# Kernel tuning notes

Measured on AMD Instinct MI355X. Metric: run time of the kernel, lower is better.

Reference implementation:

```python
import jax, jax.numpy as jnp
import numpy as np

EMBED_DIM = 768
NUM_HEADS = 12
HEAD_DIM = EMBED_DIM // NUM_HEADS  # 64


def setup_inputs() -> dict:
    key = jax.random.key(0)
    ks = jax.random.split(key, 8)
    B, T, C, H, D = 32, 512, EMBED_DIM, NUM_HEADS, HEAD_DIM
    s = 0.02
    x = jax.random.normal(ks[0], (B, T, C), dtype=jnp.float32)
    # per-head qkv: Linear(C -> 3D) stacked over heads
    Wqkv = jax.random.normal(ks[1], (H, C, 3 * D), dtype=jnp.float32) * s
    bqkv = jax.random.normal(ks[2], (H, 3 * D), dtype=jnp.float32) * s
    # per-head output proj: Linear(D -> C) stacked over heads
    Wph = jax.random.normal(ks[3], (H, D, C), dtype=jnp.float32) * s
    bph = jax.random.normal(ks[4], (H, C), dtype=jnp.float32) * s
    # final proj: Linear(H*C -> C)  (H*C == num_heads*num_heads*head_dim)
    Wproj = jax.random.normal(ks[5], (H * C, C), dtype=jnp.float32) * s
    bproj = jax.random.normal(ks[6], (C,), dtype=jnp.float32) * s
    return {"x": x, "Wqkv": Wqkv, "bqkv": bqkv, "Wph": Wph, "bph": bph,
            "Wproj": Wproj, "bproj": bproj}


def reference(x, Wqkv, bqkv, Wph, bph, Wproj, bproj):
    B, T, C = x.shape
    H, D = NUM_HEADS, HEAD_DIM
    scale = 1.0 / np.sqrt(D).astype(np.float32)
    # batched per-head qkv projection: [B,H,T,3D]
    qkv = jnp.einsum('btc,hcd->bhtd', x, Wqkv) + bqkv[None, :, None, :]
    q, k, v = jnp.split(qkv, 3, axis=-1)  # each [B,H,T,D]
    attn = jnp.einsum('bhtd,bhsd->bhts', q, k) * scale
    sa_probs = jax.nn.softmax(attn, axis=-1)  # [B,H,T,T]
    sa = jnp.einsum('bhts,bhsd->bhtd', sa_probs, v)  # [B,H,T,D]
    # per-head projection D -> C, then concat over heads (head-major order)
    heads_out = jnp.einsum('bhtd,hdc->bhtc', sa, Wph) + bph[None, :, None, :]
    cat = heads_out.transpose(0, 2, 1, 3).reshape(B, T, H * C)
    sa_out = cat @ Wproj + bproj  # [B,T,C]
    return sa_out, sa_probs
```

## Files before the change

### kernel.cpp

```cpp
#include <hip/hip_runtime.h>
#include <stdint.h>

typedef float f32x4 __attribute__((ext_vector_type(4)));
typedef short bf16x8 __attribute__((ext_vector_type(8)));

__device__ __forceinline__ unsigned short f2bf(float f) {
  union { float f; uint32_t u; } v; v.f = f;
  uint32_t r = v.u + 0x7FFFu + ((v.u >> 16) & 1u);
  return (unsigned short)(r >> 16);
}

__device__ __forceinline__ void gload16(const unsigned short* g, unsigned short* l) {
  __builtin_amdgcn_global_load_lds(
      (const __attribute__((address_space(1))) void*)g,
      (__attribute__((address_space(3))) void*)l, 16, 0, 0);
}

__global__ __launch_bounds__(256) void conv_f2b(const float* __restrict__ in,
                                                unsigned short* __restrict__ out, long n) {
  long i = ((long)blockIdx.x * 256 + threadIdx.x) * 4;
  if (i + 3 < n) {
    float4 f = *(const float4*)(in + i);
    ushort4 o;
    o.x = f2bf(f.x); o.y = f2bf(f.y); o.z = f2bf(f.z); o.w = f2bf(f.w);
    *(ushort4*)(out + i) = o;
  }
}

__global__ __launch_bounds__(256) void transpose_f2b(const float* __restrict__ in,
                                                     unsigned short* __restrict__ out,
                                                     int R, int C) {
  __shared__ unsigned short tile[32][33];
  long base = (long)blockIdx.z * R * C;
  in += base; out += base;
  int c0 = blockIdx.x * 32, r0 = blockIdx.y * 32;
  int tx = threadIdx.x & 31, ty = threadIdx.x >> 5;
#pragma unroll
  for (int i = 0; i < 32; i += 8)
    tile[ty + i][tx] = f2bf(in[(long)(r0 + ty + i) * C + c0 + tx]);
  __syncthreads();
#pragma unroll
  for (int i = 0; i < 32; i += 8)
    out[(long)(c0 + ty + i) * R + r0 + tx] = tile[tx][ty + i];
}

__global__ __launch_bounds__(256) void bias_fuse(const float* __restrict__ bph,
                                                 const float* __restrict__ Wproj,
                                                 const float* __restrict__ bproj,
                                                 float* __restrict__ bfused) {
  int j = blockIdx.x * 256 + threadIdx.x;
  int r0 = blockIdx.y * 256;
  float acc = 0.f;
  for (int r = r0; r < r0 + 256; r++)
    acc += bph[r] * Wproj[(long)r * 768 + j];
  if (blockIdx.y == 0) acc += bproj[j];
  atomicAdd(&bfused[j], acc);
}

__device__ __forceinline__ void stage8(const unsigned short* __restrict__ g,
                                       unsigned short* __restrict__ s) {
  *(uint4*)s = *(const uint4*)g;
}

template <typename AT, typename Epi>
__global__ __launch_bounds__(256) void gemm_bt(const AT* __restrict__ A, long asb, int lda,
                                               const unsigned short* __restrict__ Bt, long bsb,
                                               int ldb, int K, Epi epi) {
  __shared__ __align__(16) unsigned short As[64][32];
  __shared__ __align__(16) unsigned short Bs[64][32];
  const int tid = threadIdx.x;
  const int row = tid >> 2;
  const int kc = (tid & 3) * 8;
  const int lane = tid & 63;
  const int w = tid >> 6;
  const int quad = lane >> 4, lr = lane & 15;
  const int bz = blockIdx.z;

  f32x4 acc[4];
#pragma unroll
  for (int i = 0; i < 4; i++) acc[i] = (f32x4){0.f, 0.f, 0.f, 0.f};

  const AT* Ab = A + (long)bz * asb + (long)(blockIdx.y * 64 + row) * lda;
  const unsigned short* Bb = Bt + (long)bz * bsb + (long)(blockIdx.x * 64 + row) * ldb;

  for (int k0 = 0; k0 < K; k0 += 32) {
    stage8(Ab + k0 + kc, &As[row][kc]);
    stage8(Bb + k0 + kc, &Bs[row][kc]);
    __syncthreads();
    bf16x8 a = *(const bf16x8*)&As[w * 16 + lr][quad * 8];
#pragma unroll
    for (int nt = 0; nt < 4; nt++) {
      bf16x8 b = *(const bf16x8*)&Bs[nt * 16 + lr][quad * 8];
      acc[nt] = __builtin_amdgcn_mfma_f32_16x16x32_bf16(a, b, acc[nt], 0, 0, 0);
    }
    __syncthreads();
  }
  const int mg = blockIdx.y * 64 + w * 16 + quad * 4;
  const int ng = blockIdx.x * 64 + lr;
#pragma unroll
  for (int nt = 0; nt < 4; nt++)
#pragma unroll
    for (int r = 0; r < 4; r++)
      epi(bz, mg + r, ng + nt * 16, acc[nt][r]);
}

template <typename Epi>
__global__ __launch_bounds__(256) void gemm128(const unsigned short* __restrict__ A, int lda,
                                               const unsigned short* __restrict__ Bt, int ldb,
                                               int K, Epi epi) {
  __shared__ __align__(16) unsigned short As[128][32];
  __shared__ __align__(16) unsigned short Bs[128][32];
  const int tid = threadIdx.x;
  const int lane = tid & 63;
  const int w = tid >> 6;
  const int quad = lane >> 4, lr = lane & 15;
  const int sr = lane >> 2;
  const int sc = (lane & 3) * 8;

  f32x4 acc[4][4];
#pragma unroll
  for (int i = 0; i < 4; i++)
#pragma unroll
    for (int j = 0; j < 4; j++) acc[i][j] = (f32x4){0.f, 0.f, 0.f, 0.f};

  const unsigned short* Ag = A + (long)(blockIdx.y * 128 + w * 16 + sr) * lda + sc;
  const unsigned short* Bg = Bt + (long)(blockIdx.x * 128 + w * 16 + sr) * ldb + sc;
  unsigned short* Al0 = &As[w * 16][0];
  unsigned short* Al1 = &As[64 + w * 16][0];
  unsigned short* Bl0 = &Bs[w * 16][0];
  unsigned short* Bl1 = &Bs[64 + w * 16][0];
  const int wr = (w >> 1) * 64, wc = (w & 1) * 64;

  for (int k0 = 0; k0 < K; k0 += 32) {
    gload16(Ag + k0, Al0);
    gload16(Ag + k0 + (long)64 * lda, Al1);
    gload16(Bg + k0, Bl0);
    gload16(Bg + k0 + (long)64 * ldb, Bl1);
    __syncthreads();
    bf16x8 a[4], b[4];
#pragma unroll
    for (int mt = 0; mt < 4; mt++) a[mt] = *(const bf16x8*)&As[wr + mt * 16 + lr][quad * 8];
#pragma unroll
    for (int nt = 0; nt < 4; nt++) b[nt] = *(const bf16x8*)&Bs[wc + nt * 16 + lr][quad * 8];
#pragma unroll
    for (int mt = 0; mt < 4; mt++)
#pragma unroll
      for (int nt = 0; nt < 4; nt++)
        acc[mt][nt] = __builtin_amdgcn_mfma_f32_16x16x32_bf16(a[mt], b[nt], acc[mt][nt], 0, 0, 0);
    __syncthreads();
  }
  const int mg0 = blockIdx.y * 128 + wr + quad * 4;
  const int ng0 = blockIdx.x * 128 + wc + lr;
#pragma unroll
  for (int mt = 0; mt < 4; mt++)
#pragma unroll
    for (int nt = 0; nt < 4; nt++)
#pragma unroll
      for (int r = 0; r < 4; r++)
        epi(0, mg0 + mt * 16 + r, ng0 + nt * 16, acc[mt][nt][r]);
}

struct EpiQKV {
  const float* bqkv;
  unsigned short *q, *k, *vt;
  __device__ void operator()(int, int m, int n, float val) const {
    int h = n / 192, d3 = n - h * 192;
    unsigned short bv = f2bf(val + bqkv[n]);
    int b = m >> 9, t = m & 511;
    long bh = b * 12 + h;
    if (d3 < 64)        q[(bh * 512 + t) * 64 + d3] = bv;
    else if (d3 < 128)  k[(bh * 512 + t) * 64 + (d3 - 64)] = bv;
    else                vt[(bh * 64 + (d3 - 128)) * 512 + t] = bv;
  }
};
struct EpiWf {
  unsigned short* wft;
  __device__ void operator()(int z, int m, int n, float val) const {
    wft[(long)n * 768 + z * 64 + m] = f2bf(val);
  }
};
struct EpiOut {
  float* out;
  const float* bfused;
  __device__ void operator()(int, int m, int n, float val) const {
    out[(long)m * 768 + n] = val + bfused[n];
  }
};

__global__ __launch_bounds__(256, 2) void attn_fused(
    const unsigned short* __restrict__ q,
    const unsigned short* __restrict__ k,
    const unsigned short* __restrict__ vt,
    float* __restrict__ probs,
    unsigned short* __restrict__ sa)
{
  __shared__ __align__(16) unsigned short P[64][512];
  const int tid = threadIdx.x;
  const int w = tid >> 6;
  const int lane = tid & 63;
  const int quad = lane >> 4, lr = lane & 15;
  const int bh = blockIdx.y;
  const int q0 = blockIdx.x * 64;

  const unsigned short* Qb = q + ((long)bh * 512 + q0 + w * 16) * 64;
  const unsigned short* Kb = k + (long)bh * 512 * 64;
  const unsigned short* Vb = vt + (long)bh * 64 * 512;

  bf16x8 a0 = *(const bf16x8*)(Qb + (long)lr * 64 + quad * 8);
  bf16x8 a1 = *(const bf16x8*)(Qb + (long)lr * 64 + quad * 8 + 32);
  f32x4 acc[32];
#pragma unroll
  for (int nt = 0; nt < 32; nt++) acc[nt] = (f32x4){0.f, 0.f, 0.f, 0.f};
#pragma unroll
  for (int nt = 0; nt < 32; nt++) {
    const unsigned short* kr = Kb + (long)(nt * 16 + lr) * 64 + quad * 8;
    bf16x8 b0 = *(const bf16x8*)kr;
    bf16x8 b1 = *(const bf16x8*)(kr + 32);
    acc[nt] = __builtin_amdgcn_mfma_f32_16x16x32_bf16(a0, b0, acc[nt], 0, 0, 0);
    acc[nt] = __builtin_amdgcn_mfma_f32_16x16x32_bf16(a1, b1, acc[nt], 0, 0, 0);
  }

  float mx[4], sum[4];
#pragma unroll
  for (int r = 0; r < 4; r++) {
    float m = -1e30f;
#pragma unroll
    for (int nt = 0; nt < 32; nt++) m = fmaxf(m, acc[nt][r]);
#pragma unroll
    for (int off = 8; off; off >>= 1) m = fmaxf(m, __shfl_xor(m, off, 64));
    mx[r] = m;
    sum[r] = 0.f;
  }
#pragma unroll
  for (int nt = 0; nt < 32; nt++)
#pragma unroll
    for (int r = 0; r < 4; r++) {
      float p = __expf(0.125f * (acc[nt][r] - mx[r]));
      acc[nt][r] = p;
      sum[r] += p;
    }
#pragma unroll
  for (int r = 0; r < 4; r++) {
    float s = sum[r];
#pragma unroll
    for (int off = 8; off; off >>= 1) s += __shfl_xor(s, off, 64);
    sum[r] = 1.0f / s;
  }
  float* Pr = probs + ((long)bh * 512 + q0 + w * 16 + quad * 4) * 512 + lr;
  const int mbase = w * 16 + quad * 4;
#pragma unroll
  for (int nt = 0; nt < 32; nt++)
#pragma unroll
    for (int r = 0; r < 4; r++) {
      float p = acc[nt][r] * sum[r];
      Pr[(long)r * 512 + nt * 16] = p;
      int m = mbase + r;
      int byte = m * 1024 + (((lr + nt * 16) * 2) ^ (((m ^ (m >> 3)) & 7) << 4));
      *(unsigned short*)((char*)P + byte) = f2bf(p);
    }
  __syncthreads();

  f32x4 o[4];
#pragma unroll
  for (int dt = 0; dt < 4; dt++) o[dt] = (f32x4){0.f, 0.f, 0.f, 0.f};
  const int mrow = w * 16 + lr;
  const int swz = ((mrow ^ (mrow >> 3)) & 7) << 4;
#pragma unroll
  for (int ks = 0; ks < 16; ks++) {
    bf16x8 pa = *(const bf16x8*)((char*)P + mrow * 1024 + ((quad * 16 + ks * 64) ^ swz));
#pragma unroll
    for (int dt = 0; dt < 4; dt++) {
      bf16x8 vb = *(const bf16x8*)(Vb + (long)(dt * 16 + lr) * 512 + quad * 8 + ks * 32);
      o[dt] = __builtin_amdgcn_mfma_f32_16x16x32_bf16(pa, vb, o[dt], 0, 0, 0);
    }
  }
  const int b = bh / 12, h = bh - b * 12;
  unsigned short* So = sa + ((long)(b * 512 + q0 + w * 16 + quad * 4)) * 768 + h * 64;
#pragma unroll
  for (int dt = 0; dt < 4; dt++)
#pragma unroll
    for (int r = 0; r < 4; r++)
      So[(long)r * 768 + dt * 16 + lr] = f2bf(o[dt][r]);
}

extern "C" void kernel_launch(void* const* d_in, const int* in_sizes, int n_in,
                              void* d_out, int out_size, void* d_ws, size_t ws_size,
                              hipStream_t stream) {
  const float* x     = (const float*)d_in[0];
  const float* Wqkv  = (const float*)d_in[1];
  const float* bqkv  = (const float*)d_in[2];
  const float* Wph   = (const float*)d_in[3];
  const float* bph   = (const float*)d_in[4];
  const float* Wproj = (const float*)d_in[5];
  const float* bproj = (const float*)d_in[6];
  float* out = (float*)d_out;
  float* probs = out + 12582912L;

  char* ws = (char*)d_ws;
  auto alloc = [&](size_t bytes) {
    char* p = ws;
    ws += (bytes + 255) & ~(size_t)255;
    return p;
  };
  unsigned short* x_b    = (unsigned short*)alloc(16384L * 768 * 2);
  unsigned short* wqkvt  = (unsigned short*)alloc(2304L * 768 * 2);
  unsigned short* wph_b  = (unsigned short*)alloc(768L * 768 * 2);
  unsigned short* wprojt = (unsigned short*)alloc(768L * 9216 * 2);
  unsigned short* wft    = (unsigned short*)alloc(768L * 768 * 2);
  float*          bfused = (float*)alloc(768 * 4);
  unsigned short* qb     = (unsigned short*)alloc(12582912L * 2);
  unsigned short* kb     = (unsigned short*)alloc(12582912L * 2);
  unsigned short* vtb    = (unsigned short*)alloc(12582912L * 2);
  unsigned short* sa     = (unsigned short*)alloc(12582912L * 2);

  hipMemsetAsync(bfused, 0, 768 * 4, stream);

  conv_f2b<<<12288, 256, 0, stream>>>(x, x_b, 12582912L);
  conv_f2b<<<576, 256, 0, stream>>>(Wph, wph_b, 589824L);
  transpose_f2b<<<dim3(6, 24, 12), 256, 0, stream>>>(Wqkv, wqkvt, 768, 192);
  transpose_f2b<<<dim3(24, 288, 1), 256, 0, stream>>>(Wproj, wprojt, 9216, 768);
  bias_fuse<<<dim3(3, 36), 256, 0, stream>>>(bph, Wproj, bproj, bfused);

  gemm128<<<dim3(18, 128), 256, 0, stream>>>(x_b, 768, wqkvt, 768, 768,
                                             EpiQKV{bqkv, qb, kb, vtb});
  attn_fused<<<dim3(8, 384), 256, 0, stream>>>(qb, kb, vtb, probs, sa);
  gemm_bt<<<dim3(12, 1, 12), 256, 0, stream>>>(wph_b, 49152L, 768, wprojt, 768L, 9216, 768,
                                               EpiWf{wft});
  gemm128<<<dim3(6, 128), 256, 0, stream>>>(sa, 768, wft, 768, 768,
                                            EpiOut{out, bfused});
}
```

Baseline: 901.6 us.

## Split V projection into transposed batched GEMM and use nontemporal prob stores

The fused QKV projection is split in two. Q and K come from one GEMM with a row-major epilogue. V^T is computed directly as a batched GEMM (Wv^T times x^T per batch), so its epilogue writes contiguous rows along t instead of the strided transposed scatter used before. The fp32 softmax probability output is also written with nontemporal stores to reduce cache pollution. This adds one kernel launch and a new weight transpose layout.

```diff
diff --git a/kernel.cpp b/kernel.cpp
--- a/kernel.cpp
+++ b/kernel.cpp
@@ -42,6 +42,27 @@
 #pragma unroll
   for (int i = 0; i < 32; i += 8)
     out[(long)(c0 + ty + i) * R + r0 + tx] = tile[tx][ty + i];
+}
+
+__global__ __launch_bounds__(256) void transpose_wqkv(const float* __restrict__ in,
+                                                      unsigned short* __restrict__ wqkt,
+                                                      unsigned short* __restrict__ wvt) {
+  __shared__ unsigned short tile[32][33];
+  int h = blockIdx.z;
+  const float* src = in + (long)h * 768 * 192;
+  int c0 = blockIdx.x * 32;
+  int r0 = blockIdx.y * 32;
+  int tx = threadIdx.x & 31, ty = threadIdx.x >> 5;
+#pragma unroll
+  for (int i = 0; i < 32; i += 8)
+    tile[ty + i][tx] = f2bf(src[(long)(r0 + ty + i) * 192 + c0 + tx]);
+  __syncthreads();
+#pragma unroll
+  for (int i = 0; i < 32; i += 8) {
+    int d3 = c0 + ty + i, ch = r0 + tx;
+    if (d3 < 128) wqkt[(long)(h * 128 + d3) * 768 + ch] = tile[tx][ty + i];
+    else          wvt[(long)(h * 64 + (d3 - 128)) * 768 + ch] = tile[tx][ty + i];
+  }
 }
 
 __global__ __launch_bounds__(256) void bias_fuse(const float* __restrict__ bph,
@@ -105,9 +126,9 @@
 }
 
 template <typename Epi>
-__global__ __launch_bounds__(256) void gemm128(const unsigned short* __restrict__ A, int lda,
-                                               const unsigned short* __restrict__ Bt, int ldb,
-                                               int K, Epi epi) {
+__global__ __launch_bounds__(256) void gemm128(const unsigned short* __restrict__ A, long asb,
+                                               int lda, const unsigned short* __restrict__ Bt,
+                                               long bsb, int ldb, int K, Epi epi) {
   __shared__ __align__(16) unsigned short As[128][32];
   __shared__ __align__(16) unsigned short Bs[128][32];
   const int tid = threadIdx.x;
@@ -116,6 +137,7 @@
   const int quad = lane >> 4, lr = lane & 15;
   const int sr = lane >> 2;
   const int sc = (lane & 3) * 8;
+  const int bz = blockIdx.z;
 
   f32x4 acc[4][4];
 #pragma unroll
@@ -123,8 +145,8 @@
 #pragma unroll
     for (int j = 0; j < 4; j++) acc[i][j] = (f32x4){0.f, 0.f, 0.f, 0.f};
 
-  const unsigned short* Ag = A + (long)(blockIdx.y * 128 + w * 16 + sr) * lda + sc;
-  const unsigned short* Bg = Bt + (long)(blockIdx.x * 128 + w * 16 + sr) * ldb + sc;
+  const unsigned short* Ag = A + (long)bz * asb + (long)(blockIdx.y * 128 + w * 16 + sr) * lda + sc;
+  const unsigned short* Bg = Bt + (long)bz * bsb + (long)(blockIdx.x * 128 + w * 16 + sr) * ldb + sc;
   unsigned short* Al0 = &As[w * 16][0];
   unsigned short* Al1 = &As[64 + w * 16][0];
   unsigned short* Bl0 = &Bs[w * 16][0];
@@ -157,20 +179,26 @@
     for (int nt = 0; nt < 4; nt++)
 #pragma unroll
       for (int r = 0; r < 4; r++)
-        epi(0, mg0 + mt * 16 + r, ng0 + nt * 16, acc[mt][nt][r]);
-}
-
-struct EpiQKV {
+        epi(bz, mg0 + mt * 16 + r, ng0 + nt * 16, acc[mt][nt][r]);
+}
+
+struct EpiQK {
   const float* bqkv;
-  unsigned short *q, *k, *vt;
+  unsigned short *q, *k;
   __device__ void operator()(int, int m, int n, float val) const {
-    int h = n / 192, d3 = n - h * 192;
-    unsigned short bv = f2bf(val + bqkv[n]);
+    int h = n >> 7, d2 = n & 127;
+    unsigned short bv = f2bf(val + bqkv[h * 192 + d2]);
     int b = m >> 9, t = m & 511;
-    long bh = b * 12 + h;
-    if (d3 < 64)        q[(bh * 512 + t) * 64 + d3] = bv;
-    else if (d3 < 128)  k[(bh * 512 + t) * 64 + (d3 - 64)] = bv;
-    else                vt[(bh * 64 + (d3 - 128)) * 512 + t] = bv;
+    long base = ((long)(b * 12 + h) * 512 + t) * 64;
+    if (d2 < 64) q[base + d2] = bv;
+    else         k[base + d2 - 64] = bv;
+  }
+};
+struct EpiVt {
+  const float* bqkv;
+  unsigned short* vt;
+  __device__ void operator()(int z, int m, int n, float val) const {
+    vt[((long)z * 768 + m) * 512 + n] = f2bf(val + bqkv[(m >> 6) * 192 + 128 + (m & 63)]);
   }
 };
 struct EpiWf {
@@ -253,7 +281,7 @@
 #pragma unroll
     for (int r = 0; r < 4; r++) {
       float p = acc[nt][r] * sum[r];
-      Pr[(long)r * 512 + nt * 16] = p;
+      __builtin_nontemporal_store(p, Pr + (long)r * 512 + nt * 16);
       int m = mbase + r;
       int byte = m * 1024 + (((lr + nt * 16) * 2) ^ (((m ^ (m >> 3)) & 7) << 4));
       *(unsigned short*)((char*)P + byte) = f2bf(p);
@@ -303,7 +331,8 @@
     return p;
   };
   unsigned short* x_b    = (unsigned short*)alloc(16384L * 768 * 2);
-  unsigned short* wqkvt  = (unsigned short*)alloc(2304L * 768 * 2);
+  unsigned short* wqkt   = (unsigned short*)alloc(1536L * 768 * 2);
+  unsigned short* wvt    = (unsigned short*)alloc(768L * 768 * 2);
   unsigned short* wph_b  = (unsigned short*)alloc(768L * 768 * 2);
   unsigned short* wprojt = (unsigned short*)alloc(768L * 9216 * 2);
   unsigned short* wft    = (unsigned short*)alloc(768L * 768 * 2);
@@ -317,15 +346,17 @@
 
   conv_f2b<<<12288, 256, 0, stream>>>(x, x_b, 12582912L);
   conv_f2b<<<576, 256, 0, stream>>>(Wph, wph_b, 589824L);
-  transpose_f2b<<<dim3(6, 24, 12), 256, 0, stream>>>(Wqkv, wqkvt, 768, 192);
+  transpose_wqkv<<<dim3(6, 24, 12), 256, 0, stream>>>(Wqkv, wqkt, wvt);
   transpose_f2b<<<dim3(24, 288, 1), 256, 0, stream>>>(Wproj, wprojt, 9216, 768);
   bias_fuse<<<dim3(3, 36), 256, 0, stream>>>(bph, Wproj, bproj, bfused);
 
-  gemm128<<<dim3(18, 128), 256, 0, stream>>>(x_b, 768, wqkvt, 768, 768,
-                                             EpiQKV{bqkv, qb, kb, vtb});
+  gemm128<<<dim3(12, 128, 1), 256, 0, stream>>>(x_b, 0L, 768, wqkt, 0L, 768, 768,
+                                                EpiQK{bqkv, qb, kb});
+  gemm128<<<dim3(4, 6, 32), 256, 0, stream>>>(wvt, 0L, 768, x_b, 512L * 768, 768, 768,
+                                              EpiVt{bqkv, vtb});
   attn_fused<<<dim3(8, 384), 256, 0, stream>>>(qb, kb, vtb, probs, sa);
   gemm_bt<<<dim3(12, 1, 12), 256, 0, stream>>>(wph_b, 49152L, 768, wprojt, 768L, 9216, 768,
                                                EpiWf{wft});
-  gemm128<<<dim3(6, 128), 256, 0, stream>>>(sa, 768, wft, 768, 768,
-                                            EpiOut{out, bfused});
-}
+  gemm128<<<dim3(6, 128, 1), 256, 0, stream>>>(sa, 0L, 768, wft, 0L, 768, 768,
+                                               EpiOut{out, bfused});
+}
```

New measurement: 840.4 us. 1.07x faster.
